# Optimization experiments

Measured on AMD Instinct MI355X. Metric: run time of the kernel, lower is better.

Reference implementation:

```python
import jax, jax.numpy as jnp
import numpy as np

RES = 28          # resolution (H == W)
DIM = 384         # channels
NH = 8            # num_heads
HD = DIM // NH    # head_dim = 48
N = RES * RES     # tokens = 784
B = 16            # batch


def _build_bias_idxs(res):
    # Faithful reproduction of the first-occurrence offset indexing in __init__.
    pts = [(i, j) for i in range(res) for j in range(res)]
    offs = {}
    idxs = []
    for p1 in pts:
        for p2 in pts:
            o = (abs(p1[0] - p2[0]), abs(p1[1] - p2[1]))
            if o not in offs:
                offs[o] = len(offs)
            idxs.append(offs[o])
    return np.asarray(idxs, dtype=np.int32).reshape(res * res, res * res), len(offs)


def setup_inputs() -> dict:
    key = jax.random.key(0)
    ks = jax.random.split(key, 6)
    idxs, noff = _build_bias_idxs(RES)  # noff == RES*RES == 784
    s = 0.02
    return {
        "ll": jax.random.normal(ks[0], (B, DIM, RES, RES), jnp.float32),
        "high_attn": jax.random.normal(ks[1], (B, DIM, RES, RES), jnp.float32),
        # 1x1 convs stored as [out_ch, in_ch] matrices
        "q_w": jax.random.normal(ks[2], (DIM, DIM), jnp.float32) * s,
        "q_b": jnp.zeros((DIM,), jnp.float32),
        "kv_w": jax.random.normal(ks[3], (2 * DIM, DIM), jnp.float32) * s,
        "kv_b": jnp.zeros((2 * DIM,), jnp.float32),
        "proj_w": jax.random.normal(ks[4], (DIM, DIM), jnp.float32) * s,
        "proj_b": jnp.zeros((DIM,), jnp.float32),
        "attn_biases": jax.random.normal(ks[5], (NH, noff), jnp.float32) * s,
        "bias_idxs": jnp.asarray(idxs),  # [N, N] int32
    }


def reference(ll, high_attn, q_w, q_b, kv_w, kv_b, proj_w, proj_b, attn_biases, bias_idxs):
    b, c, h, w = ll.shape
    n = h * w
    scale = HD ** -0.5
    # 1x1 convs == per-pixel channel matmuls
    q = jnp.einsum('bchw,oc->bohw', ll, q_w) + q_b[:, None, None]
    kv = jnp.einsum('bchw,oc->bohw', high_attn, kv_w) + kv_b[:, None, None]
    k, v = jnp.split(kv, 2, axis=1)
    q = q.reshape(b, NH, HD, n).transpose(0, 1, 3, 2)  # [B,H,N,hd]
    k = k.reshape(b, NH, HD, n)                        # [B,H,hd,N]
    v = v.reshape(b, NH, HD, n).transpose(0, 1, 3, 2)  # [B,H,N,hd]
    attn = jnp.einsum('bhnd,bhdm->bhnm', q, k) * scale  # [B,H,N,N]
    bias = attn_biases[:, bias_idxs]                    # gather -> [H,N,N]
    attn = jax.nn.softmax(attn + bias[None], axis=-1)
    out = jnp.einsum('bhnm,bhmd->bhnd', attn, v)        # [B,H,N,hd]
    out = out.transpose(0, 1, 3, 2).reshape(b, c, h, w)
    return jnp.einsum('bchw,oc->bohw', out, proj_w) + proj_b[:, None, None]
```

## Files before the change

kernel.cpp:

```cpp
#include <hip/hip_runtime.h>

#define RES    28
#define DIMC   384
#define NHEAD  8
#define HDIM   48
#define DPAD   64
#define NPIX   784
#define NB     16
#define SC2    0.20823294f
#define LOG2E  1.44269504f

typedef short bf16x8 __attribute__((ext_vector_type(8)));
typedef float f32x4  __attribute__((ext_vector_type(4)));

__device__ __forceinline__ short f2bf(float x) {
  union { float f; unsigned u; } v; v.f = x;
  return (short)((v.u + 0x7FFFu + ((v.u >> 16) & 1u)) >> 16);
}
__device__ __forceinline__ unsigned pk_rne(float a, float b) {
  union { float f; unsigned u; } x, y; x.f = a; y.f = b;
  return __builtin_amdgcn_perm(y.u + 0x7FFFu + ((y.u >> 16) & 1u),
                               x.u + 0x7FFFu + ((x.u >> 16) & 1u), 0x07060302u);
}
__device__ __forceinline__ unsigned pk_hu(float a, float b) {
  union { float f; unsigned u; } x, y; x.f = a; y.f = b;
  return __builtin_amdgcn_perm(y.u + 0x8000u, x.u + 0x8000u, 0x07060302u);
}
__device__ __forceinline__ float blo(unsigned u) { union { unsigned u; float f; } v; v.u = u << 16; return v.f; }
__device__ __forceinline__ float bhi(unsigned u) { union { unsigned u; float f; } v; v.u = u & 0xFFFF0000u; return v.f; }


__global__ __launch_bounds__(256) void prep_kernel(
    const float* __restrict__ ll, const float* __restrict__ ha,
    const float* __restrict__ qw, const float* __restrict__ kvw, const float* __restrict__ pw,
    const float* __restrict__ biases,
    short* __restrict__ Xll, short* __restrict__ Xha,
    short* __restrict__ Wf2, short* __restrict__ Wfp,
    short* __restrict__ Bt3, short* __restrict__ Qb,
    short* __restrict__ Kf, short* __restrict__ Vf)
{
  __shared__ __align__(16) short sT[64][72];
  __shared__ float sB[NPIX];
  const int bid = blockIdx.x, t = threadIdx.x;

  if (bid < 2496) {
    const int px = bid % 13, cb = (bid / 13) % 6, zz = bid / 78;
    const int which = zz >> 4, b = zz & 15;
    const float* X = (which ? ha : ll) + (size_t)b * DIMC * NPIX;
    short* T = (which ? Xha : Xll);
    const int c0 = cb * 64, p0 = px * 64;
    const int rrr = t >> 4, pc = (t & 15) * 4;
#pragma unroll
    for (int i = 0; i < 4; ++i) {
      const int c = rrr + 16 * i;
      if (p0 + pc < NPIX) {
        float4 v = *(const float4*)(X + (size_t)(c0 + c) * NPIX + p0 + pc);
        sT[pc + 0][c] = f2bf(v.x); sT[pc + 1][c] = f2bf(v.y);
        sT[pc + 2][c] = f2bf(v.z); sT[pc + 3][c] = f2bf(v.w);
      }
    }
    __syncthreads();
    const int rr = t & 15, qq = (t >> 4) & 3, w = t >> 6;
    const int pxt0 = p0 >> 4, ks0 = c0 >> 5;
#pragma unroll
    for (int i = 0; i < 2; ++i) {
      const int o = w * 2 + i;
      const int pxl = o >> 1, ksl = o & 1;
      if (pxt0 + pxl < 49) {
        short* dst = T + ((size_t)(b * 49 + pxt0 + pxl) * 12 + ks0 + ksl) * 512 + (t & 63) * 8;
        *(bf16x8*)dst = *(const bf16x8*)&sT[pxl * 16 + rr][ksl * 32 + qq * 8];
      }
    }
  } else if (bid < 2784) {
    int gid = (bid - 2496) * 256 + t;
    if (gid < 55296) {
      const int lane = gid & 63;
      const int mt = (gid >> 6) & 7;
      const int ks = (gid >> 9) % 12;
      const int ct = gid / 6144;
      const int chg = ct * 128 + mt * 16 + (lane & 15);
      const int k = ks * 32 + (lane >> 4) * 8;
      const float* src = (chg < DIMC ? qw + (size_t)chg * DIMC
                                     : kvw + (size_t)(chg - DIMC) * DIMC) + k;
      const float4 a = *(const float4*)src;
      const float4 b = *(const float4*)(src + 4);
      bf16x8 o;
      o[0] = f2bf(a.x); o[1] = f2bf(a.y); o[2] = f2bf(a.z); o[3] = f2bf(a.w);
      o[4] = f2bf(b.x); o[5] = f2bf(b.y); o[6] = f2bf(b.z); o[7] = f2bf(b.w);
      *(bf16x8*)(Wf2 + (size_t)gid * 8) = o;
    } else {
      const int g2 = gid - 55296;
      const int lane = g2 & 63;
      const int ks = (g2 >> 6) % 12;
      const int mtile = g2 / 768;
      const int row = mtile * 16 + (lane & 15);
      const int k = ks * 32 + (lane >> 4) * 8;
      const float* src = pw + (size_t)row * DIMC + k;
      const float4 a = *(const float4*)src;
      const float4 b = *(const float4*)(src + 4);
      bf16x8 o;
      o[0] = f2bf(a.x); o[1] = f2bf(a.y); o[2] = f2bf(a.z); o[3] = f2bf(a.w);
      o[4] = f2bf(b.x); o[5] = f2bf(b.y); o[6] = f2bf(b.z); o[7] = f2bf(b.w);
      *(bf16x8*)(Wfp + (size_t)g2 * 8) = o;
    }
  } else if (bid < 3176) {
    const int bb = bid - 2784;
    const int h = bb / 49, qt = bb % 49;
    for (int i = t; i < NPIX; i += 256) sB[i] = biases[h * NPIX + i] * LOG2E;
    __syncthreads();
    const int rr = t & 15, qq = (t >> 4) & 3, w = t >> 6;
    const int qrow = qt * 16 + rr;
    const int i2 = qrow / RES, j2 = qrow - i2 * RES;
    short* dst0 = Bt3 + ((size_t)(h * 49 + qt) * 25) * 512 + (t & 63) * 8;
    const short NEG = f2bf(-1e30f);
    for (int c = w; c < 25; c += 4) {
      short v8[8];
#pragma unroll
      for (int hf = 0; hf < 2; ++hf)
#pragma unroll
        for (int u = 0; u < 4; ++u) {
          const int k = c * 32 + hf * 16 + qq * 4 + u;
          if (k < NPIX) {
            const int i1 = k / RES, j1 = k - i1 * RES;
            int di = i1 - i2; di = di < 0 ? -di : di;
            int dj = j1 - j2; dj = dj < 0 ? -dj : dj;
            v8[hf * 4 + u] = f2bf(sB[di * RES + dj]);
          } else v8[hf * 4 + u] = NEG;
        }
      *(bf16x8*)(dst0 + (size_t)c * 512) = *(const bf16x8*)v8;
    }
  } else {
    const int pp = bid - 3176;
    if (pp < 392) {
      const size_t r = (size_t)pp * 256 + t;
      short* p = Qb + r * DPAD + HDIM;
      *(int4*)p = make_int4(0, 0, 0, 0);
      *(int4*)(p + 8) = make_int4(0, 0, 0, 0);
    } else if (pp < 1192) {
      const int id = (pp - 392) * 256 + t;
      const int l32 = id & 31;
      const int frag = 1 + 2 * ((id >> 5) & 1);
      const int chunk = (id >> 6) % 25;
      const int bh2 = id / 1600;
      short* dst = Kf + (((size_t)bh2 * 25 + chunk) * 4 + frag) * 512 + (32 + l32) * 8;
      *(int4*)dst = make_int4(0, 0, 0, 0);
    } else if (pp < 1256) {
      const int id = (pp - 1192) * 256 + t;
      const int lane2 = id & 63;
      const int frag = 2 + ((id >> 6) & 1);
      const int bh2 = id >> 7;
      short* dst = Kf + (((size_t)bh2 * 25 + 24) * 4 + frag) * 512 + lane2 * 8;
      *(int4*)dst = make_int4(0, 0, 0, 0);
    } else {
      const int id = (pp - 1256) * 256 + t;
      const int bh2 = id / 96;
      const int rem = id - bh2 * 96;
      const int frag = rem >> 5;
      const int l32 = rem & 31;
      short* dst = Vf + (((size_t)bh2 * 25 + 24) * 3 + frag) * 512 + (32 + l32) * 8;
      *(int4*)dst = make_int4(0, 0, 0, 0);
    }
  }
}

__global__ __launch_bounds__(256) void qkv_tiled(
    const short* __restrict__ Wf2, const float* __restrict__ qb, const float* __restrict__ kvb,
    const short* __restrict__ Xll, const short* __restrict__ Xha,
    short* __restrict__ Qb, short* __restrict__ Kf, short* __restrict__ Vf)
{
  __shared__ __align__(16) short sM[15360];
  const int t = threadIdx.x;
  const int w = t >> 6, lane = t & 63;
  const int rr = lane & 15, qq = lane >> 4;
  const int ct = blockIdx.x;
  const int pt = blockIdx.y;
  const int b = pt / 7, pt7 = pt % 7;
  const int px0 = pt7 * 112;

  const short* Xsel = (ct < 3 ? Xll : Xha);
  const int xt0 = b * 49 + pt7 * 7;

  const short* Ap = Wf2 + (size_t)ct * 12 * 4096 + 2 * w * 512 + lane * 8;

  f32x4 acc[2][7];
#pragma unroll
  for (int mi = 0; mi < 2; ++mi)
#pragma unroll
    for (int pg = 0; pg < 7; ++pg) acc[mi][pg] = (f32x4){0.f, 0.f, 0.f, 0.f};

  auto stageB = [&](int buf, int s) {
    short* l0 = &sM[buf * 3584 + w * 512];
    const short* g0 = Xsel + ((size_t)(xt0 + w) * 12 + s) * 512 + lane * 8;
    __builtin_amdgcn_global_load_lds((const __attribute__((address_space(1))) void*)g0,
                                     (__attribute__((address_space(3))) void*)l0, 16, 0, 0);
    if (w < 3) {
      short* l1 = &sM[buf * 3584 + (w + 4) * 512];
      const short* g1 = Xsel + ((size_t)(xt0 + w + 4) * 12 + s) * 512 + lane * 8;
      __builtin_amdgcn_global_load_lds((const __attribute__((address_space(1))) void*)g1,
                                       (__attribute__((address_space(3))) void*)l1, 16, 0, 0);
    }
  };

  stageB(0, 0);
  bf16x8 a0c = *(const bf16x8*)(Ap);
  bf16x8 a1c = *(const bf16x8*)(Ap + 512);
  __syncthreads();

  for (int s = 0; s < 12; ++s) {
    const int buf = s & 1;
    if (s < 11) stageB(buf ^ 1, s + 1);
    const int sn = s < 11 ? s + 1 : s;
    const short* an = Ap + (size_t)sn * 4096;
    const bf16x8 a0n = *(const bf16x8*)(an);
    const bf16x8 a1n = *(const bf16x8*)(an + 512);

    const short* sBb = &sM[buf * 3584];
#pragma unroll
    for (int pg = 0; pg < 7; ++pg) {
      const bf16x8 bf = *(const bf16x8*)(sBb + pg * 512 + lane * 8);
      acc[0][pg] = __builtin_amdgcn_mfma_f32_16x16x32_bf16(a0c, bf, acc[0][pg], 0, 0, 0);
      acc[1][pg] = __builtin_amdgcn_mfma_f32_16x16x32_bf16(a1c, bf, acc[1][pg], 0, 0, 0);
    }
    a0c = a0n; a1c = a1n;
    __syncthreads();
  }

  if (ct < 3) {
#pragma unroll
    for (int mi = 0; mi < 2; ++mi) {
      const int ch = ct * 128 + (2 * w + mi) * 16 + qq * 4;
      const float4 bv = *(const float4*)(qb + ch);
      const int hh = ch / HDIM, d0 = ch % HDIM;
#pragma unroll
      for (int pg = 0; pg < 7; ++pg) {
        const int px = px0 + pg * 16 + rr;
        uint2 pk;
        pk.x = pk_rne(acc[mi][pg][0] + bv.x, acc[mi][pg][1] + bv.y);
        pk.y = pk_rne(acc[mi][pg][2] + bv.z, acc[mi][pg][3] + bv.w);
        *(uint2*)(Qb + (((size_t)b * NHEAD + hh) * NPIX + px) * DPAD + d0) = pk;
      }
    }
  } else if (ct < 6) {
#pragma unroll
    for (int mi = 0; mi < 2; ++mi) {
      const int ch = (ct - 3) * 128 + (2 * w + mi) * 16 + qq * 4;
      const float4 bv = *(const float4*)(kvb + ch);
      const int hh = ch / HDIM, dq = ch % HDIM;
      const int fd = dq >> 5;
      const int laneHi = (dq & 31) >> 3;
      const int elo = dq & 7;
#pragma unroll
      for (int pg = 0; pg < 7; ++pg) {
        const int px = px0 + pg * 16 + rr;
        const int chunk = px >> 5, kh = (px >> 4) & 1;
        uint2 pk;
        pk.x = pk_rne(acc[mi][pg][0] + bv.x, acc[mi][pg][1] + bv.y);
        pk.y = pk_rne(acc[mi][pg][2] + bv.z, acc[mi][pg][3] + bv.w);
        short* dst = Kf + ((((size_t)b * NHEAD + hh) * 25 + chunk) * 4 + kh * 2 + fd) * 512
                     + ((px & 15) + (laneHi << 4)) * 8 + elo;
        *(uint2*)dst = pk;
      }
    }
  } else {
#pragma unroll
    for (int mi = 0; mi < 2; ++mi) {
      const int chl = (2 * w + mi) * 16 + qq * 4;
      const int chv = (ct - 6) * 128 + chl;
      const float4 bv = *(const float4*)(kvb + DIMC + chv);
      const float bb[4] = {bv.x, bv.y, bv.z, bv.w};
#pragma unroll
      for (int pg = 0; pg < 7; ++pg) {
        const int px = pg * 16 + rr;
#pragma unroll
        for (int j = 0; j < 4; ++j)
          sM[(chl + j) * 120 + px] = f2bf(acc[mi][pg][j] + bb[j]);
      }
    }
    __syncthreads();
    for (int id = t; id < 1792; id += 256) {
      const int r = id / 14, o = id - r * 14;
      const int k = px0 + o * 8;
      const int chunk = k >> 5, qv = (k >> 3) & 3;
      const int chv = (ct - 6) * 128 + r;
      const int hh = chv / HDIM, d = chv % HDIM;
      short* dst = Vf + ((((size_t)b * NHEAD + hh) * 25 + chunk) * 3 + (d >> 4)) * 512
                   + ((d & 15) + (qv << 4)) * 8;
      *(bf16x8*)dst = *(const bf16x8*)&sM[r * 120 + o * 8];
    }
  }
}

struct Chain { float sp; f32x4 O0, O1, O2; };

__device__ __forceinline__ void chain_init(Chain& c) {
  c.sp = 0.f;
  c.O0 = (f32x4){0.f,0.f,0.f,0.f}; c.O1 = c.O0; c.O2 = c.O0;
}

__device__ __forceinline__ void chain_step(
    Chain& c, const f32x4 d0, const f32x4 d1, const uint2 bw0, const uint2 bw1,
    short* sPt, const int rr, const int qq)
{
  float s[8];
  s[0] = fmaf(d0[0], SC2, blo(bw0.x)); s[1] = fmaf(d0[1], SC2, bhi(bw0.x));
  s[2] = fmaf(d0[2], SC2, blo(bw0.y)); s[3] = fmaf(d0[3], SC2, bhi(bw0.y));
  s[4] = fmaf(d1[0], SC2, blo(bw1.x)); s[5] = fmaf(d1[1], SC2, bhi(bw1.x));
  s[6] = fmaf(d1[2], SC2, blo(bw1.y)); s[7] = fmaf(d1[3], SC2, bhi(bw1.y));
  float p[8];
#pragma unroll
  for (int j = 0; j < 8; ++j) p[j] = exp2f(s[j]);
  const float ss = ((p[0] + p[1]) + (p[2] + p[3])) + ((p[4] + p[5]) + (p[6] + p[7]));
  c.sp += ss;
  uint2 w0; w0.x = pk_hu(p[0], p[1]); w0.y = pk_hu(p[2], p[3]);
  uint2 w1; w1.x = pk_hu(p[4], p[5]); w1.y = pk_hu(p[6], p[7]);
  *(uint2*)(sPt + rr * 40 + qq * 4) = w0;
  *(uint2*)(sPt + rr * 40 + 16 + qq * 4) = w1;
}

__global__ __launch_bounds__(256) void attn_kernel(
    const short* __restrict__ Q, const short* __restrict__ Kf,
    const short* __restrict__ Vf, const short* __restrict__ Bt3,
    short* __restrict__ AOf)
{
  __shared__ __align__(16) char sMem[20480];
  short* sPbase = (short*)sMem;
  const int t = threadIdx.x;
  const int w = t >> 6, lane = t & 63;
  const int rr = lane & 15, qq = lane >> 4;
  const int x = blockIdx.x;
  const int h = x & 7;
  const int i = x >> 3;
  const int b = i / 25, qt = i - b * 25;
  const int qA = qt * 32;
  const bool hasB = (qA + 16 < NPIX);
  const int bh = b * NHEAD + h;

  const short* QpA = Q + ((size_t)bh * NPIX + qA + rr) * DPAD + qq * 8;
  const short* QpB = Q + ((size_t)bh * NPIX + (hasB ? qA + 16 : qA) + rr) * DPAD + qq * 8;
  const bf16x8 qfA0 = *(const bf16x8*)QpA;
  const bf16x8 qfA1 = *(const bf16x8*)(QpA + 32);
  const bf16x8 qfB0 = *(const bf16x8*)QpB;
  const bf16x8 qfB1 = *(const bf16x8*)(QpB + 32);

  const short* Kfp = Kf + (size_t)bh * (25 * 4 * 512) + lane * 8;
  const short* Vfp = Vf + (size_t)bh * (25 * 3 * 512) + lane * 8;
  const short* BpA = Bt3 + ((size_t)(h * 49 + 2 * qt) * 25) * 512 + lane * 8;
  const short* BpB = Bt3 + ((size_t)(h * 49 + (hasB ? 2 * qt + 1 : 2 * qt)) * 25) * 512 + lane * 8;
  short* sPA = sPbase + (w * 2 + 0) * 640;
  short* sPB = sPbase + (w * 2 + 1) * 640;

  Chain cA, cB;
  chain_init(cA); chain_init(cB);

  const int cbeg = w * 6;
  const int cend = (w == 3) ? 25 : cbeg + 6;

  for (int c = cbeg; c < cend; ++c) {
    const short* kc = Kfp + (size_t)c * 2048;
    const bf16x8 ka0 = *(const bf16x8*)kc;
    const bf16x8 ka1 = *(const bf16x8*)(kc + 512);
    const bf16x8 kb0 = *(const bf16x8*)(kc + 1024);
    const bf16x8 kb1 = *(const bf16x8*)(kc + 1536);

    f32x4 dA0 = (f32x4){0.f,0.f,0.f,0.f}, dA1 = dA0, dB0 = dA0, dB1 = dA0;
    __builtin_amdgcn_s_setprio(1);
    dA0 = __builtin_amdgcn_mfma_f32_16x16x32_bf16(ka0, qfA0, dA0, 0, 0, 0);
    dA0 = __builtin_amdgcn_mfma_f32_16x16x32_bf16(ka1, qfA1, dA0, 0, 0, 0);
    dB0 = __builtin_amdgcn_mfma_f32_16x16x32_bf16(ka0, qfB0, dB0, 0, 0, 0);
    dB0 = __builtin_amdgcn_mfma_f32_16x16x32_bf16(ka1, qfB1, dB0, 0, 0, 0);
    dA1 = __builtin_amdgcn_mfma_f32_16x16x32_bf16(kb0, qfA0, dA1, 0, 0, 0);
    dA1 = __builtin_amdgcn_mfma_f32_16x16x32_bf16(kb1, qfA1, dA1, 0, 0, 0);
    dB1 = __builtin_amdgcn_mfma_f32_16x16x32_bf16(kb0, qfB0, dB1, 0, 0, 0);
    dB1 = __builtin_amdgcn_mfma_f32_16x16x32_bf16(kb1, qfB1, dB1, 0, 0, 0);
    __builtin_amdgcn_s_setprio(0);

    const uint4 bA = *(const uint4*)(BpA + (size_t)c * 512);
    const uint4 bB = *(const uint4*)(BpB + (size_t)c * 512);

    chain_step(cA, dA0, dA1, make_uint2(bA.x, bA.y), make_uint2(bA.z, bA.w), sPA, rr, qq);
    chain_step(cB, dB0, dB1, make_uint2(bB.x, bB.y), make_uint2(bB.z, bB.w), sPB, rr, qq);

    const short* vc = Vfp + (size_t)c * 1536;
    const bf16x8 vf0 = *(const bf16x8*)vc;
    const bf16x8 vf1 = *(const bf16x8*)(vc + 512);
    const bf16x8 vf2 = *(const bf16x8*)(vc + 1024);
    const bf16x8 pfA = *(const bf16x8*)(sPA + rr * 40 + qq * 8);
    const bf16x8 pfB = *(const bf16x8*)(sPB + rr * 40 + qq * 8);
    __builtin_amdgcn_s_setprio(1);
    cA.O0 = __builtin_amdgcn_mfma_f32_16x16x32_bf16(vf0, pfA, cA.O0, 0, 0, 0);
    cA.O1 = __builtin_amdgcn_mfma_f32_16x16x32_bf16(vf1, pfA, cA.O1, 0, 0, 0);
    cA.O2 = __builtin_amdgcn_mfma_f32_16x16x32_bf16(vf2, pfA, cA.O2, 0, 0, 0);
    cB.O0 = __builtin_amdgcn_mfma_f32_16x16x32_bf16(vf0, pfB, cB.O0, 0, 0, 0);
    cB.O1 = __builtin_amdgcn_mfma_f32_16x16x32_bf16(vf1, pfB, cB.O1, 0, 0, 0);
    cB.O2 = __builtin_amdgcn_mfma_f32_16x16x32_bf16(vf2, pfB, cB.O2, 0, 0, 0);
    __builtin_amdgcn_s_setprio(0);
  }

  __syncthreads();
  float* mbuf = (float*)sMem;
  if (w > 0) {
    const int col = ((w - 1) * 2 + 0) * 64 + lane;
    const int colB = col + 64;
    float vals[13] = {cA.O0[0], cA.O0[1], cA.O0[2], cA.O0[3],
                      cA.O1[0], cA.O1[1], cA.O1[2], cA.O1[3],
                      cA.O2[0], cA.O2[1], cA.O2[2], cA.O2[3], cA.sp};
    float valsB[13] = {cB.O0[0], cB.O0[1], cB.O0[2], cB.O0[3],
                       cB.O1[0], cB.O1[1], cB.O1[2], cB.O1[3],
                       cB.O2[0], cB.O2[1], cB.O2[2], cB.O2[3], cB.sp};
#pragma unroll
    for (int j = 0; j < 13; ++j) mbuf[j * 384 + col] = vals[j];
#pragma unroll
    for (int j = 0; j < 13; ++j) mbuf[j * 384 + colB] = valsB[j];
  }
  __syncthreads();
  if (w != 0) return;

#pragma unroll
  for (int ww = 0; ww < 3; ++ww) {
    const int col = (ww * 2 + 0) * 64 + lane;
    const int colB = col + 64;
#pragma unroll
    for (int j = 0; j < 4; ++j) {
      cA.O0[j] += mbuf[j * 384 + col];
      cA.O1[j] += mbuf[(4 + j) * 384 + col];
      cA.O2[j] += mbuf[(8 + j) * 384 + col];
      cB.O0[j] += mbuf[j * 384 + colB];
      cB.O1[j] += mbuf[(4 + j) * 384 + colB];
      cB.O2[j] += mbuf[(8 + j) * 384 + colB];
    }
    cA.sp += mbuf[12 * 384 + col];
    cB.sp += mbuf[12 * 384 + colB];
  }

  {
    float sA = cA.sp;
    sA += __shfl_xor(sA, 16); sA += __shfl_xor(sA, 32);
    const float invA = 1.f / sA;
    const f32x4 OA[3] = {cA.O0, cA.O1, cA.O2};
    short* base = AOf + ((size_t)(b * 49 + 2 * qt) * 12) * 512;
#pragma unroll
    for (int part = 0; part < 3; ++part) {
      const int ch = h * HDIM + part * 16 + qq * 4;
      uint2 pk;
      pk.x = pk_rne(OA[part][0] * invA, OA[part][1] * invA);
      pk.y = pk_rne(OA[part][2] * invA, OA[part][3] * invA);
      short* dst = base + (ch >> 5) * 512 + (rr + (((ch >> 3) & 3) << 4)) * 8 + (ch & 7);
      *(uint2*)dst = pk;
    }
  }
  if (hasB) {
    float sB2 = cB.sp;
    sB2 += __shfl_xor(sB2, 16); sB2 += __shfl_xor(sB2, 32);
    const float invB = 1.f / sB2;
    const f32x4 OB[3] = {cB.O0, cB.O1, cB.O2};
    short* base = AOf + ((size_t)(b * 49 + 2 * qt + 1) * 12) * 512;
#pragma unroll
    for (int part = 0; part < 3; ++part) {
      const int ch = h * HDIM + part * 16 + qq * 4;
      uint2 pk;
      pk.x = pk_rne(OB[part][0] * invB, OB[part][1] * invB);
      pk.y = pk_rne(OB[part][2] * invB, OB[part][3] * invB);
      short* dst = base + (ch >> 5) * 512 + (rr + (((ch >> 3) & 3) << 4)) * 8 + (ch & 7);
      *(uint2*)dst = pk;
    }
  }
}

__global__ __launch_bounds__(256) void proj_gemm(
    const short* __restrict__ Wfp, const float* __restrict__ pb,
    const short* __restrict__ AOf, float* __restrict__ out)
{
  const int t = threadIdx.x;
  const int w = t >> 6, lane = t & 63;
  const int rr = lane & 15, qq = lane >> 4;
  const int b = blockIdx.y;
  const int bx = blockIdx.x;
  const int pix = bx * 16 + rr;

  const short* Xp = AOf + ((size_t)(b * 49 + bx) * 12) * 512 + lane * 8;
  const short* wfp = Wfp + ((size_t)w * 12 * 64 + lane) * 8;

  f32x4 acc[6];
#pragma unroll
  for (int i = 0; i < 6; ++i) acc[i] = (f32x4){0.f, 0.f, 0.f, 0.f};

  bf16x8 xfc = *(const bf16x8*)(Xp);
  bf16x8 afc[6];
#pragma unroll
  for (int i = 0; i < 6; ++i) afc[i] = *(const bf16x8*)(wfp + (size_t)i * 24576);

#pragma unroll 2
  for (int ks = 0; ks < 12; ++ks) {
    const int kn = ks + (ks < 11 ? 1 : 0);
    const bf16x8 xfn = *(const bf16x8*)(Xp + kn * 512);
    bf16x8 afn[6];
#pragma unroll
    for (int i = 0; i < 6; ++i)
      afn[i] = *(const bf16x8*)(wfp + (size_t)i * 24576 + kn * 512);

#pragma unroll
    for (int i = 0; i < 6; ++i)
      acc[i] = __builtin_amdgcn_mfma_f32_16x16x32_bf16(afc[i], xfc, acc[i], 0, 0, 0);

    xfc = xfn;
#pragma unroll
    for (int i = 0; i < 6; ++i) afc[i] = afn[i];
  }
#pragma unroll
  for (int i = 0; i < 6; ++i) {
    const int ch0 = (w + 4 * i) * 16 + qq * 4;
    const float4 bv = *(const float4*)(pb + ch0);
    float* o = out + ((size_t)b * DIMC + ch0) * NPIX + pix;
    o[0] = acc[i][0] + bv.x;
    o[NPIX] = acc[i][1] + bv.y;
    o[2 * NPIX] = acc[i][2] + bv.z;
    o[3 * NPIX] = acc[i][3] + bv.w;
  }
}

extern "C" void kernel_launch(void* const* d_in, const int* in_sizes, int n_in,
                              void* d_out, int out_size, void* d_ws, size_t ws_size,
                              hipStream_t stream)
{
  const float* ll     = (const float*)d_in[0];
  const float* ha     = (const float*)d_in[1];
  const float* q_w    = (const float*)d_in[2];
  const float* q_b    = (const float*)d_in[3];
  const float* kv_w   = (const float*)d_in[4];
  const float* kv_b   = (const float*)d_in[5];
  const float* proj_w = (const float*)d_in[6];
  const float* proj_b = (const float*)d_in[7];
  const float* biases = (const float*)d_in[8];
  float* out = (float*)d_out;

  short* Qb  = (short*)d_ws;
  short* Kf  = Qb  + (size_t)NB * NHEAD * NPIX * DPAD;
  short* Vf  = Kf  + (size_t)128 * 25 * 4 * 512;
  short* Xll = Vf  + (size_t)128 * 25 * 3 * 512;
  short* Xha = Xll + (size_t)NB * 49 * 12 * 512;
  short* AOf = Xha + (size_t)NB * 49 * 12 * 512;
  short* Bt3 = AOf + (size_t)NB * 49 * 12 * 512;
  short* Wf2 = Bt3 + (size_t)NHEAD * 49 * 25 * 512;
  short* Wfp = Wf2 + (size_t)55296 * 8;

  prep_kernel<<<dim3(4480), 256, 0, stream>>>(ll, ha, q_w, kv_w, proj_w, biases,
                                              Xll, Xha, Wf2, Wfp, Bt3, Qb, Kf, Vf);
  qkv_tiled<<<dim3(9, 112), 256, 0, stream>>>(Wf2, q_b, kv_b, Xll, Xha, Qb, Kf, Vf);
  attn_kernel<<<dim3(3200), 256, 0, stream>>>(Qb, Kf, Vf, Bt3, AOf);
  proj_gemm<<<dim3(49, NB), 256, 0, stream>>>(Wfp, proj_b, AOf, out);
}
```

Before: 193.8 us.

## Fold scale into Q, seed QK accumulators with bias, compute row sums via MFMA

The softmax scale (including log2e) is now folded into Q at projection time, and the bias tile is loaded first and used as the initial accumulator of the QK MFMAs. This removes the per-element FMA and bias unpacking after the matmul. Row sums of P are computed by an extra MFMA against a ones vector instead of scalar adds and cross-lane shuffles, and P packing uses the hardware v_cvt_pk_bf16_f32 instruction. The trade is two extra MFMAs per chunk and row sums taken from bf16-rounded P, which changes numerics slightly.

```diff
diff --git a/kernel.cpp b/kernel.cpp
--- a/kernel.cpp
+++ b/kernel.cpp
@@ -22,9 +22,10 @@
   return __builtin_amdgcn_perm(y.u + 0x7FFFu + ((y.u >> 16) & 1u),
                                x.u + 0x7FFFu + ((x.u >> 16) & 1u), 0x07060302u);
 }
-__device__ __forceinline__ unsigned pk_hu(float a, float b) {
-  union { float f; unsigned u; } x, y; x.f = a; y.f = b;
-  return __builtin_amdgcn_perm(y.u + 0x8000u, x.u + 0x8000u, 0x07060302u);
+__device__ __forceinline__ unsigned cvtpk(float a, float b) {
+  unsigned r;
+  asm("v_cvt_pk_bf16_f32 %0, %1, %2" : "=v"(r) : "v"(a), "v"(b));
+  return r;
 }
 __device__ __forceinline__ float blo(unsigned u) { union { unsigned u; float f; } v; v.u = u << 16; return v.f; }
 __device__ __forceinline__ float bhi(unsigned u) { union { unsigned u; float f; } v; v.u = u & 0xFFFF0000u; return v.f; }
@@ -235,8 +236,8 @@
       for (int pg = 0; pg < 7; ++pg) {
         const int px = px0 + pg * 16 + rr;
         uint2 pk;
-        pk.x = pk_rne(acc[mi][pg][0] + bv.x, acc[mi][pg][1] + bv.y);
-        pk.y = pk_rne(acc[mi][pg][2] + bv.z, acc[mi][pg][3] + bv.w);
+        pk.x = pk_rne((acc[mi][pg][0] + bv.x) * SC2, (acc[mi][pg][1] + bv.y) * SC2);
+        pk.y = pk_rne((acc[mi][pg][2] + bv.z) * SC2, (acc[mi][pg][3] + bv.w) * SC2);
         *(uint2*)(Qb + (((size_t)b * NHEAD + hh) * NPIX + px) * DPAD + d0) = pk;
       }
     }
@@ -292,27 +293,13 @@
 
 struct Chain { float sp; f32x4 O0, O1, O2; };
 
-__device__ __forceinline__ void chain_init(Chain& c) {
-  c.sp = 0.f;
-  c.O0 = (f32x4){0.f,0.f,0.f,0.f}; c.O1 = c.O0; c.O2 = c.O0;
-}
-
-__device__ __forceinline__ void chain_step(
-    Chain& c, const f32x4 d0, const f32x4 d1, const uint2 bw0, const uint2 bw1,
-    short* sPt, const int rr, const int qq)
+__device__ __forceinline__ void store_p(
+    const f32x4 d0, const f32x4 d1, short* sPt, const int rr, const int qq)
 {
-  float s[8];
-  s[0] = fmaf(d0[0], SC2, blo(bw0.x)); s[1] = fmaf(d0[1], SC2, bhi(bw0.x));
-  s[2] = fmaf(d0[2], SC2, blo(bw0.y)); s[3] = fmaf(d0[3], SC2, bhi(bw0.y));
-  s[4] = fmaf(d1[0], SC2, blo(bw1.x)); s[5] = fmaf(d1[1], SC2, bhi(bw1.x));
-  s[6] = fmaf(d1[2], SC2, blo(bw1.y)); s[7] = fmaf(d1[3], SC2, bhi(bw1.y));
-  float p[8];
-#pragma unroll
-  for (int j = 0; j < 8; ++j) p[j] = exp2f(s[j]);
-  const float ss = ((p[0] + p[1]) + (p[2] + p[3])) + ((p[4] + p[5]) + (p[6] + p[7]));
-  c.sp += ss;
-  uint2 w0; w0.x = pk_hu(p[0], p[1]); w0.y = pk_hu(p[2], p[3]);
-  uint2 w1; w1.x = pk_hu(p[4], p[5]); w1.y = pk_hu(p[6], p[7]);
+  const float p0 = exp2f(d0[0]), p1 = exp2f(d0[1]), p2 = exp2f(d0[2]), p3 = exp2f(d0[3]);
+  const float p4 = exp2f(d1[0]), p5 = exp2f(d1[1]), p6 = exp2f(d1[2]), p7 = exp2f(d1[3]);
+  uint2 w0; w0.x = cvtpk(p0, p1); w0.y = cvtpk(p2, p3);
+  uint2 w1; w1.x = cvtpk(p4, p5); w1.y = cvtpk(p6, p7);
   *(uint2*)(sPt + rr * 40 + qq * 4) = w0;
   *(uint2*)(sPt + rr * 40 + 16 + qq * 4) = w1;
 }
@@ -349,20 +336,31 @@
   short* sPA = sPbase + (w * 2 + 0) * 640;
   short* sPB = sPbase + (w * 2 + 1) * 640;
 
+  const bf16x8 onesf = {(short)0x3F80, (short)0x3F80, (short)0x3F80, (short)0x3F80,
+                        (short)0x3F80, (short)0x3F80, (short)0x3F80, (short)0x3F80};
+
   Chain cA, cB;
-  chain_init(cA); chain_init(cB);
+  cA.O0 = (f32x4){0.f,0.f,0.f,0.f}; cA.O1 = cA.O0; cA.O2 = cA.O0;
+  cB.O0 = cA.O0; cB.O1 = cA.O0; cB.O2 = cA.O0;
+  f32x4 spA = cA.O0, spB = cA.O0;
 
   const int cbeg = w * 6;
   const int cend = (w == 3) ? 25 : cbeg + 6;
 
   for (int c = cbeg; c < cend; ++c) {
+    const uint4 bA = *(const uint4*)(BpA + (size_t)c * 512);
+    const uint4 bB = *(const uint4*)(BpB + (size_t)c * 512);
     const short* kc = Kfp + (size_t)c * 2048;
     const bf16x8 ka0 = *(const bf16x8*)kc;
     const bf16x8 ka1 = *(const bf16x8*)(kc + 512);
     const bf16x8 kb0 = *(const bf16x8*)(kc + 1024);
     const bf16x8 kb1 = *(const bf16x8*)(kc + 1536);
 
-    f32x4 dA0 = (f32x4){0.f,0.f,0.f,0.f}, dA1 = dA0, dB0 = dA0, dB1 = dA0;
+    f32x4 dA0 = (f32x4){blo(bA.x), bhi(bA.x), blo(bA.y), bhi(bA.y)};
+    f32x4 dA1 = (f32x4){blo(bA.z), bhi(bA.z), blo(bA.w), bhi(bA.w)};
+    f32x4 dB0 = (f32x4){blo(bB.x), bhi(bB.x), blo(bB.y), bhi(bB.y)};
+    f32x4 dB1 = (f32x4){blo(bB.z), bhi(bB.z), blo(bB.w), bhi(bB.w)};
+
     __builtin_amdgcn_s_setprio(1);
     dA0 = __builtin_amdgcn_mfma_f32_16x16x32_bf16(ka0, qfA0, dA0, 0, 0, 0);
     dA0 = __builtin_amdgcn_mfma_f32_16x16x32_bf16(ka1, qfA1, dA0, 0, 0, 0);
@@ -374,11 +372,8 @@
     dB1 = __builtin_amdgcn_mfma_f32_16x16x32_bf16(kb1, qfB1, dB1, 0, 0, 0);
     __builtin_amdgcn_s_setprio(0);
 
-    const uint4 bA = *(const uint4*)(BpA + (size_t)c * 512);
-    const uint4 bB = *(const uint4*)(BpB + (size_t)c * 512);
-
-    chain_step(cA, dA0, dA1, make_uint2(bA.x, bA.y), make_uint2(bA.z, bA.w), sPA, rr, qq);
-    chain_step(cB, dB0, dB1, make_uint2(bB.x, bB.y), make_uint2(bB.z, bB.w), sPB, rr, qq);
+    store_p(dA0, dA1, sPA, rr, qq);
+    store_p(dB0, dB1, sPB, rr, qq);
 
     const short* vc = Vfp + (size_t)c * 1536;
     const bf16x8 vf0 = *(const bf16x8*)vc;
@@ -390,11 +385,15 @@
     cA.O0 = __builtin_amdgcn_mfma_f32_16x16x32_bf16(vf0, pfA, cA.O0, 0, 0, 0);
     cA.O1 = __builtin_amdgcn_mfma_f32_16x16x32_bf16(vf1, pfA, cA.O1, 0, 0, 0);
     cA.O2 = __builtin_amdgcn_mfma_f32_16x16x32_bf16(vf2, pfA, cA.O2, 0, 0, 0);
+    spA   = __builtin_amdgcn_mfma_f32_16x16x32_bf16(onesf, pfA, spA, 0, 0, 0);
     cB.O0 = __builtin_amdgcn_mfma_f32_16x16x32_bf16(vf0, pfB, cB.O0, 0, 0, 0);
     cB.O1 = __builtin_amdgcn_mfma_f32_16x16x32_bf16(vf1, pfB, cB.O1, 0, 0, 0);
     cB.O2 = __builtin_amdgcn_mfma_f32_16x16x32_bf16(vf2, pfB, cB.O2, 0, 0, 0);
+    spB   = __builtin_amdgcn_mfma_f32_16x16x32_bf16(onesf, pfB, spB, 0, 0, 0);
     __builtin_amdgcn_s_setprio(0);
   }
+  cA.sp = spA[0];
+  cB.sp = spB[0];
 
   __syncthreads();
   float* mbuf = (float*)sMem;
@@ -433,9 +432,7 @@
   }
 
   {
-    float sA = cA.sp;
-    sA += __shfl_xor(sA, 16); sA += __shfl_xor(sA, 32);
-    const float invA = 1.f / sA;
+    const float invA = 1.f / cA.sp;
     const f32x4 OA[3] = {cA.O0, cA.O1, cA.O2};
     short* base = AOf + ((size_t)(b * 49 + 2 * qt) * 12) * 512;
 #pragma unroll
@@ -449,9 +446,7 @@
     }
   }
   if (hasB) {
-    float sB2 = cB.sp;
-    sB2 += __shfl_xor(sB2, 16); sB2 += __shfl_xor(sB2, 32);
-    const float invB = 1.f / sB2;
+    const float invB = 1.f / cB.sp;
     const f32x4 OB[3] = {cB.O0, cB.O1, cB.O2};
     short* base = AOf + ((size_t)(b * 49 + 2 * qt + 1) * 12) * 512;
 #pragma unroll
```

Result: no change. 194.8 us (+0.5%).
